# Kernel tuning notes

Hardware: AMD Instinct MI355X
Metric: run time of the kernel (lower is better)

The kernel has to match this reference:

```python
import jax, jax.numpy as jnp
import numpy as np

N_NODES = 100000
DIM_IN = 128
DIM_H = 64
LATENT = 64
N_EDGES = 1200000


def setup_inputs() -> dict:
    key = jax.random.key(0)
    ks = jax.random.split(key, 8)
    x = jax.random.normal(ks[0], (N_NODES, DIM_IN), dtype=jnp.float32)
    edge_index = jax.random.randint(ks[1], (2, N_EDGES), 0, N_NODES, dtype=jnp.int32)
    batch = jnp.zeros((N_NODES,), dtype=jnp.int32)
    s_in = 1.0 / np.sqrt(DIM_IN)
    s_h = 1.0 / np.sqrt(DIM_H)
    gcn_w = jax.random.uniform(ks[2], (DIM_IN, DIM_H), jnp.float32, -s_in, s_in)
    gcn_b = jnp.zeros((DIM_H,), dtype=jnp.float32)
    w1 = jax.random.uniform(ks[3], (DIM_H, LATENT), jnp.float32, -s_h, s_h)
    b1 = jax.random.uniform(ks[4], (LATENT,), jnp.float32, -s_h, s_h)
    s_l = 1.0 / np.sqrt(LATENT)
    w3 = jax.random.uniform(ks[5], (LATENT, LATENT), jnp.float32, -s_l, s_l)
    b3 = jax.random.uniform(ks[6], (LATENT,), jnp.float32, -s_l, s_l)
    return {"x": x, "edge_index": edge_index, "batch": batch,
            "gcn_w": gcn_w, "gcn_b": gcn_b, "w1": w1, "b1": b1, "w3": w3, "b3": b3}


def _gcn_conv(x, edge_index, W, b):
    n = x.shape[0]
    loop = jnp.arange(n, dtype=edge_index.dtype)
    src = jnp.concatenate([edge_index[0], loop])
    dst = jnp.concatenate([edge_index[1], loop])
    deg = jax.ops.segment_sum(jnp.ones_like(dst, dtype=x.dtype), dst, num_segments=n)
    dinv = jnp.where(deg > 0, jax.lax.rsqrt(deg), 0.0)
    norm = dinv[src] * dinv[dst]                      # [E+N]
    h = x @ W                                          # [N, dim_h]
    msg = h[src] * norm[:, None]                       # gather + scale
    out = jax.ops.segment_sum(msg, dst, num_segments=n)  # scatter-add
    return out + b


def reference(x, edge_index, batch, gcn_w, gcn_b, w1, b1, w3, b3):
    g1 = _gcn_conv(x, edge_index, gcn_w, gcn_b)
    l1 = g1 @ w1 + b1
    l3 = l1 @ w3 + b3
    # mu/sigma/z/kl in the original are side effects not returned; output is l3
    return l3
```

## Files before the change

kernel.cpp:

```cpp
#include <hip/hip_runtime.h>
#include <hip/hip_bf16.h>

#define N_NODES 100000
#define N_EDGES 1200000
#define NBK 256
#define NPB 391
#define CAPB 5376
#define EPB 4096
#define BIN_BLKS 293
#define XW_BLKS 1280
#define FUSED_GRID (BIN_BLKS + XW_BLKS)

typedef __attribute__((ext_vector_type(8))) short bf16x8;
typedef __attribute__((ext_vector_type(4))) float f32x4;

__global__ __launch_bounds__(256) void k_w(const float* __restrict__ gcn_w,
                                           const float* __restrict__ gcn_b,
                                           const float* __restrict__ w1,
                                           const float* __restrict__ b1,
                                           const float* __restrict__ w3,
                                           const float* __restrict__ b3,
                                           short* __restrict__ WcB,
                                           float* __restrict__ bc,
                                           int* __restrict__ bcnt) {
    __shared__ float tmp[4096];
    __shared__ float tb[64];
    const int b = blockIdx.x, t = threadIdx.x;
    if (b == 31 && t < NBK) bcnt[t] = 0;
    if (b == 0 && t < 64) {
        float s = b1[t];
        for (int k = 0; k < 64; ++k) s = fmaf(gcn_b[k], w1[k * 64 + t], s);
        tb[t] = s;
    }
    for (int i = t; i < 4096; i += 256) {
        const int r = i >> 6, c = i & 63;
        float a = 0.f;
#pragma unroll 8
        for (int k = 0; k < 64; ++k) a = fmaf(w1[r * 64 + k], w3[k * 64 + c], a);
        tmp[i] = a;
    }
    __syncthreads();
    const int i = b * 256 + t;
    const int r = i >> 6, c = i & 63;
    float a = 0.f;
#pragma unroll 8
    for (int k = 0; k < 64; ++k) a = fmaf(gcn_w[r * 64 + k], tmp[k * 64 + c], a);
    const int kt = r >> 5, kr = r & 31, g = kr >> 3, e = kr & 7;
    const int ct = c & 3, cl = c >> 2, lane = g * 16 + cl;
    WcB[(((kt * 4 + ct) * 64) + lane) * 8 + e] =
        __builtin_bit_cast(short, __float2bfloat16(a));
    if (b == 0 && t < 64) {
        float s = b3[t];
        for (int k = 0; k < 64; ++k) s = fmaf(tb[k], w3[k * 64 + t], s);
        bc[t] = s;
    }
}

__global__ __launch_bounds__(256) void k_fused(const int* __restrict__ ei,
                                               int* __restrict__ bcnt,
                                               int* __restrict__ binned,
                                               const float* __restrict__ x,
                                               const short* __restrict__ WcB,
                                               unsigned char* __restrict__ hsq,
                                               float* __restrict__ hscale) {
    const int b = blockIdx.x;
    if (b < BIN_BLKS) {
        __shared__ int hist[NBK], base[NBK], cur[NBK];
        const int t = threadIdx.x;
        const int e0 = b * EPB;
        for (int i = t; i < NBK; i += 256) hist[i] = 0;
        __syncthreads();
        for (int j = t; j < EPB; j += 256) {
            const int e = e0 + j;
            if (e < N_EDGES) atomicAdd(&hist[ei[N_EDGES + e] / NPB], 1);
        }
        __syncthreads();
        for (int i = t; i < NBK; i += 256) {
            const int h = hist[i];
            base[i] = h ? atomicAdd(&bcnt[i], h) : 0;
            cur[i] = 0;
        }
        __syncthreads();
        for (int j = t; j < EPB; j += 256) {
            const int e = e0 + j;
            if (e < N_EDGES) {
                const int s = ei[e];
                const int d = ei[N_EDGES + e];
                const int bk = d / NPB;
                const int dl = d - bk * NPB;
                const int p = base[bk] + atomicAdd(&cur[bk], 1);
                if (p < CAPB) binned[bk * CAPB + p] = s | (dl << 17);
            }
        }
    } else {
        const int t = threadIdx.x, w = t >> 6, lane = t & 63;
        const int cl = lane & 15, g = lane >> 4;
        bf16x8 bfrag[16];
#pragma unroll
        for (int f = 0; f < 16; ++f) bfrag[f] = ((const bf16x8*)WcB)[f * 64 + lane];

        const int ntiles = N_NODES / 16;
        const int nw = XW_BLKS * 4;
        for (int tile = (b - BIN_BLKS) * 4 + w; tile < ntiles; tile += nw) {
            const int node0 = tile * 16;
            const float* xrow = x + (size_t)(node0 + cl) * 128 + g * 8;
            f32x4 xa[4][2];
#pragma unroll
            for (int kt = 0; kt < 4; ++kt) {
                xa[kt][0] = *(const f32x4*)(xrow + kt * 32);
                xa[kt][1] = *(const f32x4*)(xrow + kt * 32 + 4);
            }
            f32x4 acc[4];
#pragma unroll
            for (int ct = 0; ct < 4; ++ct) acc[ct] = (f32x4){0.f, 0.f, 0.f, 0.f};
#pragma unroll
            for (int kt = 0; kt < 4; ++kt) {
                bf16x8 af;
#pragma unroll
                for (int j = 0; j < 4; ++j) {
                    af[j]     = __builtin_bit_cast(short, __float2bfloat16(xa[kt][0][j]));
                    af[j + 4] = __builtin_bit_cast(short, __float2bfloat16(xa[kt][1][j]));
                }
#pragma unroll
                for (int ct = 0; ct < 4; ++ct)
                    acc[ct] = __builtin_amdgcn_mfma_f32_16x16x32_bf16(
                        af, bfrag[kt * 4 + ct], acc[ct], 0, 0, 0);
            }
            float mx[4];
#pragma unroll
            for (int j = 0; j < 4; ++j) {
                mx[j] = fmaxf(fmaxf(fabsf(acc[0][j]), fabsf(acc[1][j])),
                              fmaxf(fabsf(acc[2][j]), fabsf(acc[3][j])));
            }
#pragma unroll
            for (int m = 1; m < 16; m <<= 1)
#pragma unroll
                for (int j = 0; j < 4; ++j)
                    mx[j] = fmaxf(mx[j], __shfl_xor(mx[j], m));
#pragma unroll
            for (int j = 0; j < 4; ++j) {
                const float sc = fmaxf(mx[j], 1e-20f) * (1.f / 127.f);
                const float inv = 127.f / fmaxf(mx[j], 1e-20f);
                unsigned int pk = 0;
#pragma unroll
                for (int ct = 0; ct < 4; ++ct) {
                    const int v = (int)rintf(acc[ct][j] * inv);
                    pk |= ((unsigned int)(v & 0xFF)) << (8 * ct);
                }
                *(unsigned int*)(hsq + (size_t)(node0 + g * 4 + j) * 64 + cl * 4) = pk;
                if (cl == j) hscale[node0 + g * 4 + j] = sc;
            }
        }
    }
}

__global__ __launch_bounds__(512) void k_csr(const int* __restrict__ bcnt,
                                             const int* __restrict__ binned,
                                             const float* __restrict__ hscale,
                                             int* __restrict__ csr,
                                             int* __restrict__ rowptr,
                                             int* __restrict__ degA,
                                             float* __restrict__ dinv,
                                             float* __restrict__ csca) {
    __shared__ int stage[CAPB];
    __shared__ int sdeg[NPB], sloc[NPB], scur[NPB];
    const int b = blockIdx.x, t = threadIdx.x;
    const int m = min(bcnt[b], CAPB);
    for (int i = t; i < NPB; i += 512) { sdeg[i] = 0; scur[i] = 0; }
    __syncthreads();
    for (int j = t; j < m; j += 512) {
        const int pk = binned[b * CAPB + j];
        stage[j] = pk;
        atomicAdd(&sdeg[pk >> 17], 1);
    }
    __syncthreads();
    if (t < 64) {
        int run = 0;
#pragma unroll
        for (int c0 = 0; c0 < NPB; c0 += 64) {
            const int idx = c0 + t;
            const int v = (idx < NPB) ? sdeg[idx] : 0;
            int inc = v;
#pragma unroll
            for (int o = 1; o < 64; o <<= 1) {
                const int u = __shfl_up(inc, o);
                if (t >= o) inc += u;
            }
            if (idx < NPB) sloc[idx] = run + inc - v;
            run += __shfl(inc, 63);
        }
    }
    __syncthreads();
    for (int i = t; i < NPB; i += 512) {
        const int node = b * NPB + i;
        if (node < N_NODES) {
            const int v = sdeg[i];
            const float dv = rsqrtf((float)(v + 1));
            rowptr[node] = b * CAPB + sloc[i];
            degA[node] = v;
            dinv[node] = dv;
            csca[node] = dv * hscale[node];
        }
    }
    for (int j = t; j < m; j += 512) {
        const int pk = stage[j];
        const int dl = pk >> 17;
        const int p = atomicAdd(&scur[dl], 1);
        csr[b * CAPB + sloc[dl] + p] = pk & 0x1FFFF;
    }
}

__global__ __launch_bounds__(512) void k_gather(const int* __restrict__ rowptr,
                                                const int* __restrict__ degA,
                                                const int* __restrict__ csr,
                                                const unsigned char* __restrict__ hsq,
                                                const float* __restrict__ csca,
                                                const float* __restrict__ dinv,
                                                const float* __restrict__ bc,
                                                float* __restrict__ out) {
    const int t = threadIdx.x, wave = t >> 6, lane = t & 63;
    const int node = blockIdx.x * 8 + wave;
    const int deg = degA[node];
    const int base = rowptr[node];
    const float dvn = dinv[node];
    const float csN = csca[node];
    const int cl = lane & 15, g = lane >> 4;
    const int cc = cl * 4;
    const unsigned int qs = *(const unsigned int*)(hsq + (size_t)node * 64 + cc);

    f32x4 acc = (f32x4){0.f, 0.f, 0.f, 0.f};
    for (int j0 = 0; j0 < deg; j0 += 64) {
        const int rem = min(deg - j0, 64);
        int s_l = 0;
        float c_l = 0.f;
        if (lane < rem) {
            s_l = csr[base + j0 + lane];
            c_l = csca[s_l];
        }
        for (int i0 = 0; i0 < rem; i0 += 16) {
#pragma unroll
            for (int u = 0; u < 4; ++u) {
                const int jj = i0 + u * 4 + g;
                const int sj = __shfl(s_l, jj);
                const float cj = __shfl(c_l, jj);
                if (jj < rem) {
                    const unsigned int q =
                        *(const unsigned int*)(hsq + (size_t)sj * 64 + cc);
                    acc[0] = fmaf((float)(int)(signed char)(q & 0xFFu), cj, acc[0]);
                    acc[1] = fmaf((float)(int)(signed char)((q >> 8) & 0xFFu), cj, acc[1]);
                    acc[2] = fmaf((float)(int)(signed char)((q >> 16) & 0xFFu), cj, acc[2]);
                    acc[3] = fmaf((float)(int)(signed char)(q >> 24), cj, acc[3]);
                }
            }
        }
    }
#pragma unroll
    for (int k = 0; k < 4; ++k) {
        acc[k] += __shfl_xor(acc[k], 16);
        acc[k] += __shfl_xor(acc[k], 32);
    }
    const float4 bc4 = *(const float4*)(bc + cc);
    float4 res;
    res.x = fmaf(fmaf((float)(int)(signed char)(qs & 0xFFu), csN, acc[0]), dvn, bc4.x);
    res.y = fmaf(fmaf((float)(int)(signed char)((qs >> 8) & 0xFFu), csN, acc[1]), dvn, bc4.y);
    res.z = fmaf(fmaf((float)(int)(signed char)((qs >> 16) & 0xFFu), csN, acc[2]), dvn, bc4.z);
    res.w = fmaf(fmaf((float)(int)(signed char)(qs >> 24), csN, acc[3]), dvn, bc4.w);
    if (g == 0) *(float4*)(out + (size_t)node * 64 + cc) = res;
}

extern "C" void kernel_launch(void* const* d_in, const int* in_sizes, int n_in,
                              void* d_out, int out_size, void* d_ws, size_t ws_size,
                              hipStream_t stream) {
    const float* x     = (const float*)d_in[0];
    const int*   ei    = (const int*)d_in[1];
    const float* gcn_w = (const float*)d_in[3];
    const float* gcn_b = (const float*)d_in[4];
    const float* w1    = (const float*)d_in[5];
    const float* b1    = (const float*)d_in[6];
    const float* w3    = (const float*)d_in[7];
    const float* b3    = (const float*)d_in[8];
    float* out = (float*)d_out;

    char* ws = (char*)d_ws;
    int*           bcnt   = (int*)(ws);
    short*         WcB    = (short*)(ws + 1024);
    float*         bc     = (float*)(ws + 17408);
    float*         dinv   = (float*)(ws + 17664);
    int*           rowptr = (int*)(ws + 417664);
    int*           degA   = (int*)(ws + 817664);
    float*         hscale = (float*)(ws + 1217664);
    float*         csca   = (float*)(ws + 1617664);
    unsigned char* hsq    = (unsigned char*)(ws + 2017664);
    int*           binned = (int*)(ws + 8417664);
    int*           csr    = (int*)(ws + 13922688);

    k_w<<<32, 256, 0, stream>>>(gcn_w, gcn_b, w1, b1, w3, b3, WcB, bc, bcnt);
    k_fused<<<FUSED_GRID, 256, 0, stream>>>(ei, bcnt, binned, x, WcB, hsq, hscale);
    k_csr<<<NBK, 512, 0, stream>>>(bcnt, binned, hscale, csr, rowptr, degA, dinv, csca);
    k_gather<<<N_NODES / 8, 512, 0, stream>>>(rowptr, degA, csr, hsq, csca,
                                              dinv, bc, out);
}
```

Baseline: 114.6 us.

## Make gather kernel persistent with software-pipelined prefetch of next nodes' metadata

Turns the one-wave-per-node gather kernel into a persistent grid of 2048 blocks of 4 waves, each wave looping over nodes with a stride. While aggregating the current node, it prefetches the next node's degree, row pointer, scale factors and first CSR chunk, and the metadata for the node after that. The aim is to hide the dependent load latency chain (degA/rowptr -> csr -> csca -> hsq) and cut block launch overhead. In exchange it raises register pressure and gives less parallelism per wave.

```diff
diff --git a/kernel.cpp b/kernel.cpp
--- a/kernel.cpp
+++ b/kernel.cpp
@@ -10,6 +10,7 @@
 #define BIN_BLKS 293
 #define XW_BLKS 1280
 #define FUSED_GRID (BIN_BLKS + XW_BLKS)
+#define GB 2048
 
 typedef __attribute__((ext_vector_type(8))) short bf16x8;
 typedef __attribute__((ext_vector_type(4))) float f32x4;
@@ -210,7 +211,7 @@
     }
 }
 
-__global__ __launch_bounds__(512) void k_gather(const int* __restrict__ rowptr,
+__global__ __launch_bounds__(256) void k_gather(const int* __restrict__ rowptr,
                                                 const int* __restrict__ degA,
                                                 const int* __restrict__ csr,
                                                 const unsigned char* __restrict__ hsq,
@@ -218,34 +219,49 @@
                                                 const float* __restrict__ dinv,
                                                 const float* __restrict__ bc,
                                                 float* __restrict__ out) {
-    const int t = threadIdx.x, wave = t >> 6, lane = t & 63;
-    const int node = blockIdx.x * 8 + wave;
-    const int deg = degA[node];
-    const int base = rowptr[node];
-    const float dvn = dinv[node];
-    const float csN = csca[node];
-    const int cl = lane & 15, g = lane >> 4;
-    const int cc = cl * 4;
-    const unsigned int qs = *(const unsigned int*)(hsq + (size_t)node * 64 + cc);
-
-    f32x4 acc = (f32x4){0.f, 0.f, 0.f, 0.f};
-    for (int j0 = 0; j0 < deg; j0 += 64) {
-        const int rem = min(deg - j0, 64);
-        int s_l = 0;
-        float c_l = 0.f;
-        if (lane < rem) {
-            s_l = csr[base + j0 + lane];
-            c_l = csca[s_l];
-        }
-        for (int i0 = 0; i0 < rem; i0 += 16) {
+    const int t = threadIdx.x, wv = t >> 6, lane = t & 63;
+    const int cl = lane & 15, g = lane >> 4, cc = cl * 4;
+    const int NW = GB * 4;
+    int n = blockIdx.x * 4 + wv;
+    const float4 bc4 = *(const float4*)(bc + cc);
+
+    int deg0 = degA[n], base0 = rowptr[n];
+    float dvn0 = dinv[n], csn0 = csca[n];
+    unsigned qs0 = *(const unsigned*)(hsq + (size_t)n * 64 + cc);
+    int s0 = 0; float c0 = 0.f;
+    {
+        const int r = min(deg0, 64);
+        if (lane < r) { s0 = csr[base0 + lane]; c0 = csca[s0]; }
+    }
+    int n1 = n + NW;
+    int deg1 = 0, base1 = 0; float dvn1 = 0.f, csn1 = 0.f; unsigned qs1 = 0;
+    if (n1 < N_NODES) {
+        deg1 = degA[n1]; base1 = rowptr[n1];
+        dvn1 = dinv[n1]; csn1 = csca[n1];
+        qs1 = *(const unsigned*)(hsq + (size_t)n1 * 64 + cc);
+    }
+
+    for (;;) {
+        const int r1 = min(deg1, 64);
+        int s1 = 0;
+        if (n1 < N_NODES && lane < r1) s1 = csr[base1 + lane];
+        const int n2 = n1 + NW;
+        int deg2 = 0, base2 = 0; float dvn2 = 0.f, csn2 = 0.f; unsigned qs2 = 0;
+        if (n2 < N_NODES) {
+            deg2 = degA[n2]; base2 = rowptr[n2];
+            dvn2 = dinv[n2]; csn2 = csca[n2];
+            qs2 = *(const unsigned*)(hsq + (size_t)n2 * 64 + cc);
+        }
+        f32x4 acc = (f32x4){0.f, 0.f, 0.f, 0.f};
+        const int r0 = min(deg0, 64);
+        for (int i0 = 0; i0 < r0; i0 += 16) {
 #pragma unroll
             for (int u = 0; u < 4; ++u) {
                 const int jj = i0 + u * 4 + g;
-                const int sj = __shfl(s_l, jj);
-                const float cj = __shfl(c_l, jj);
-                if (jj < rem) {
-                    const unsigned int q =
-                        *(const unsigned int*)(hsq + (size_t)sj * 64 + cc);
+                const int sj = __shfl(s0, jj);
+                const float cj = __shfl(c0, jj);
+                if (jj < r0) {
+                    const unsigned q = *(const unsigned*)(hsq + (size_t)sj * 64 + cc);
                     acc[0] = fmaf((float)(int)(signed char)(q & 0xFFu), cj, acc[0]);
                     acc[1] = fmaf((float)(int)(signed char)((q >> 8) & 0xFFu), cj, acc[1]);
                     acc[2] = fmaf((float)(int)(signed char)((q >> 16) & 0xFFu), cj, acc[2]);
@@ -253,19 +269,45 @@
                 }
             }
         }
-    }
-#pragma unroll
-    for (int k = 0; k < 4; ++k) {
-        acc[k] += __shfl_xor(acc[k], 16);
-        acc[k] += __shfl_xor(acc[k], 32);
-    }
-    const float4 bc4 = *(const float4*)(bc + cc);
-    float4 res;
-    res.x = fmaf(fmaf((float)(int)(signed char)(qs & 0xFFu), csN, acc[0]), dvn, bc4.x);
-    res.y = fmaf(fmaf((float)(int)(signed char)((qs >> 8) & 0xFFu), csN, acc[1]), dvn, bc4.y);
-    res.z = fmaf(fmaf((float)(int)(signed char)((qs >> 16) & 0xFFu), csN, acc[2]), dvn, bc4.z);
-    res.w = fmaf(fmaf((float)(int)(signed char)(qs >> 24), csN, acc[3]), dvn, bc4.w);
-    if (g == 0) *(float4*)(out + (size_t)node * 64 + cc) = res;
+        for (int j0 = 64; j0 < deg0; j0 += 64) {
+            const int rem = min(deg0 - j0, 64);
+            int sl = 0; float clv = 0.f;
+            if (lane < rem) { sl = csr[base0 + j0 + lane]; clv = csca[sl]; }
+            for (int i0 = 0; i0 < rem; i0 += 16) {
+#pragma unroll
+                for (int u = 0; u < 4; ++u) {
+                    const int jj = i0 + u * 4 + g;
+                    const int sj = __shfl(sl, jj);
+                    const float cj = __shfl(clv, jj);
+                    if (jj < rem) {
+                        const unsigned q = *(const unsigned*)(hsq + (size_t)sj * 64 + cc);
+                        acc[0] = fmaf((float)(int)(signed char)(q & 0xFFu), cj, acc[0]);
+                        acc[1] = fmaf((float)(int)(signed char)((q >> 8) & 0xFFu), cj, acc[1]);
+                        acc[2] = fmaf((float)(int)(signed char)((q >> 16) & 0xFFu), cj, acc[2]);
+                        acc[3] = fmaf((float)(int)(signed char)(q >> 24), cj, acc[3]);
+                    }
+                }
+            }
+        }
+#pragma unroll
+        for (int k = 0; k < 4; ++k) {
+            acc[k] += __shfl_xor(acc[k], 16);
+            acc[k] += __shfl_xor(acc[k], 32);
+        }
+        float4 res;
+        res.x = fmaf(fmaf((float)(int)(signed char)(qs0 & 0xFFu), csn0, acc[0]), dvn0, bc4.x);
+        res.y = fmaf(fmaf((float)(int)(signed char)((qs0 >> 8) & 0xFFu), csn0, acc[1]), dvn0, bc4.y);
+        res.z = fmaf(fmaf((float)(int)(signed char)((qs0 >> 16) & 0xFFu), csn0, acc[2]), dvn0, bc4.z);
+        res.w = fmaf(fmaf((float)(int)(signed char)(qs0 >> 24), csn0, acc[3]), dvn0, bc4.w);
+        if (g == 0) *(float4*)(out + (size_t)n * 64 + cc) = res;
+
+        if (n1 >= N_NODES) break;
+        float c1 = 0.f;
+        if (lane < r1) c1 = csca[s1];
+        n = n1; deg0 = deg1; base0 = base1; dvn0 = dvn1; csn0 = csn1;
+        qs0 = qs1; s0 = s1; c0 = c1;
+        n1 = n2; deg1 = deg2; base1 = base2; dvn1 = dvn2; csn1 = csn2; qs1 = qs2;
+    }
 }
 
 extern "C" void kernel_launch(void* const* d_in, const int* in_sizes, int n_in,
@@ -297,6 +339,5 @@
     k_w<<<32, 256, 0, stream>>>(gcn_w, gcn_b, w1, b1, w3, b3, WcB, bc, bcnt);
     k_fused<<<FUSED_GRID, 256, 0, stream>>>(ei, bcnt, binned, x, WcB, hsq, hscale);
     k_csr<<<NBK, 512, 0, stream>>>(bcnt, binned, hscale, csr, rowptr, degA, dinv, csca);
-    k_gather<<<N_NODES / 8, 512, 0, stream>>>(rowptr, degA, csr, hsq, csca,
-                                              dinv, bc, out);
-}
+    k_gather<<<GB, 256, 0, stream>>>(rowptr, degA, csr, hsq, csca, dinv, bc, out);
+}
```

Measured after the change: 102.3 us. -10.8%, faster.
